# Optimization experiments

Hardware: AMD Instinct MI355X
Metric: run time of the kernel (lower is better)

## Reference

```python
import jax, jax.numpy as jnp
import numpy as np

NEG_INF = -1e9  # matches torch masked_fill value of -1000000000.0


def setup_inputs() -> dict:
    key = jax.random.key(0)
    k1, k2, k3, k4 = jax.random.split(key, 4)
    B, H, S, D = 4, 16, 2048, 128
    query = jax.random.normal(k1, (B, H, S, D), dtype=jnp.float32)
    key_t = jax.random.normal(k2, (B, H, S, D), dtype=jnp.float32)
    value = jax.random.normal(k3, (B, H, S, D), dtype=jnp.float32)
    mask = jax.random.randint(k4, (B, 1, 1, S), 0, 2, dtype=jnp.int32)
    return {"query": query, "key": key_t, "value": value, "mask": mask, "dropout": 0}


def reference(query, key, value, mask, dropout):
    # scores = Q K^T / sqrt(d_k)   [B,H,S,S]
    d_k = query.shape[-1]
    scores = jnp.einsum("bhqd,bhkd->bhqk", query, key) / jnp.sqrt(jnp.asarray(d_k, query.dtype))
    # masked_fill_(mask == 0, -1e9); mask broadcasts [B,1,1,S] -> [B,H,S,S]
    scores = jnp.where(mask == 0, jnp.asarray(NEG_INF, scores.dtype), scores)
    # dropout == 0 -> identity (deterministic reference / eval mode)
    attn = jax.nn.softmax(scores, axis=-1)
    return jnp.einsum("bhqk,bhkd->bhqd", attn, value)
```

## Files before the change

kernel.cpp:

```cpp
#include <hip/hip_runtime.h>
#include <hip/hip_bf16.h>

#define S_LEN 2048
#define D_DIM 128
#define QBLK 128
#define KVBLK 32
#define NT (S_LEN / KVBLK)
#define KCHUNK 8192
#define VCHUNK 8192
#define PRE_BYTES ((size_t)64 * NT * (KCHUNK + VCHUNK))

typedef __attribute__((ext_vector_type(8))) short short8v;
typedef __attribute__((ext_vector_type(16))) float f32x16;

static __device__ __forceinline__ unsigned f2bf2(float lo, float hi) {
    float2 f2; f2.x = lo; f2.y = hi;
    __hip_bfloat162 h2 = __float22bfloat162_rn(f2);
    unsigned r;
    __builtin_memcpy(&r, &h2, 4);
    return r;
}

static __device__ __forceinline__ void plswap(unsigned& a, unsigned& b) {
    auto r = __builtin_amdgcn_permlane32_swap(a, b, false, false);
    a = r[0]; b = r[1];
}
static __device__ __forceinline__ float plswap_sum(float x) {
    unsigned a = __float_as_uint(x), b = a;
    plswap(a, b);
    return __uint_as_float(a) + __uint_as_float(b);
}

static __device__ __forceinline__ void gload16(const void* g, void* l) {
    __builtin_amdgcn_global_load_lds(
        (const __attribute__((address_space(1))) unsigned int*)g,
        (__attribute__((address_space(3))) unsigned int*)l,
        16, 0, 0);
}

static __device__ __forceinline__ void stage8k(const unsigned char* g, unsigned char* l,
                                               int wv, int lane) {
#pragma unroll
    for (int i = 0; i < 2; ++i) {
        const int off = (wv * 2 + i) * 1024;
        gload16(g + off + lane * 16, l + off);
    }
}

#define VTS 133

__global__ __launch_bounds__(256) void preconv(
    const float* __restrict__ Kp, const float* __restrict__ Vp,
    unsigned short* __restrict__ Ko, unsigned short* __restrict__ Vo)
{
    __shared__ float vt[64 * VTS];
    const int tid = threadIdx.x;
    const int blk = blockIdx.x;
    const size_t gbase = (size_t)(blk >> 5) * S_LEN * D_DIM + (size_t)(blk & 31) * 64 * D_DIM;

#pragma unroll
    for (int i = 0; i < 8; ++i) {
        int idx = (tid + 256 * i) * 4;
        int row = idx >> 7, col = idx & 127;
        float4 v4 = *(const float4*)(Vp + gbase + idx);
        float* d = &vt[row * VTS + col];
        d[0] = v4.x; d[1] = v4.y; d[2] = v4.z; d[3] = v4.w;
    }

    unsigned short* kout = Ko + (size_t)blk * 8192;
#pragma unroll
    for (int i = 0; i < 4; ++i) {
        int o = tid + 256 * i;
        int row = o >> 4, bs = o & 15;
        int b = (bs & 8) | ((bs ^ row) & 7);
        const float* gp = Kp + gbase + row * D_DIM + 8 * b;
        float4 x = *(const float4*)gp;
        float4 y = *(const float4*)(gp + 4);
        uint4 w;
        w.x = f2bf2(x.x, x.y); w.y = f2bf2(x.z, x.w);
        w.z = f2bf2(y.x, y.y); w.w = f2bf2(y.z, y.w);
        *(uint4*)(kout + o * 8) = w;
    }
    __syncthreads();

    unsigned short* vout = Vo + (size_t)blk * 8192;
#pragma unroll
    for (int i = 0; i < 4; ++i) {
        int u = tid + 256 * i;
        int ch = u >> 9, r = u & 511;
        int d = r >> 2, bs = r & 3;
        int b = bs ^ ((d >> 1) & 3);
        const float* c0 = &vt[(ch * 32 + 8 * b) * VTS + d];
        uint4 w;
        w.x = f2bf2(c0[0 * VTS], c0[1 * VTS]);
        w.y = f2bf2(c0[2 * VTS], c0[3 * VTS]);
        w.z = f2bf2(c0[4 * VTS], c0[5 * VTS]);
        w.w = f2bf2(c0[6 * VTS], c0[7 * VTS]);
        *(uint4*)(vout + u * 8) = w;
    }
}

#define ASMEM (16384 + 16384 + 8192)

__global__ __launch_bounds__(256, 4) void sdpa_fwd_pre(
    const float* __restrict__ Qp, const unsigned short* __restrict__ Kpre,
    const unsigned short* __restrict__ Vpre, const int* __restrict__ Mp,
    float* __restrict__ Op)
{
    extern __shared__ unsigned char smem[];
    unsigned char* KbB = smem;
    unsigned char* VbB = smem + 16384;
    float* blds = (float*)(smem + 32768);

    const int tid  = threadIdx.x;
    const int lane = tid & 63;
    const int wv   = tid >> 6;
    const int h    = lane >> 5;
    const int c31  = lane & 31;
    const int hrx  = h ^ (c31 & 7);
    const int vsx  = (c31 >> 1) & 3;
    const int lbid = ((blockIdx.x & 7) << 7) | (blockIdx.x >> 3);
    const int bh   = lbid >> 4;
    const int q0   = (lbid & 15) * QBLK;
    const int bb   = bh >> 4;
    const size_t base = (size_t)bh * S_LEN * D_DIM;
    const unsigned char* Kg = (const unsigned char*)Kpre + (size_t)bh * (NT * KCHUNK);
    const unsigned char* Vg = (const unsigned char*)Vpre + (size_t)bh * (NT * VCHUNK);

    constexpr float SC   = 0.08838834764831845f * 1.4426950408889634f;
    constexpr float NEGB = -1.4426950408889634e9f;
    constexpr float M2   = 16.0f;

    {
        const int* mp = Mp + bb * S_LEN;
#pragma unroll
        for (int i = 0; i < S_LEN / 256; ++i)
            blds[tid + 256 * i] = mp[tid + 256 * i] ? -M2 : NEGB;
    }

    short8v qf[8];
    {
        const float* qrp = Qp + base + (size_t)(q0 + 32 * wv + c31) * D_DIM;
#pragma unroll
        for (int kk = 0; kk < 8; ++kk) {
            float4 x = *(const float4*)(qrp + 16 * kk + 8 * h);
            float4 y = *(const float4*)(qrp + 16 * kk + 8 * h + 4);
            uint4 w;
            w.x = f2bf2(x.x * SC, x.y * SC); w.y = f2bf2(x.z * SC, x.w * SC);
            w.z = f2bf2(y.x * SC, y.y * SC); w.w = f2bf2(y.z * SC, y.w * SC);
            *(uint4*)&qf[kk] = w;
        }
    }

    stage8k(Kg, KbB, wv, lane);
    stage8k(Vg, VbB, wv, lane);
    __syncthreads();

    f32x16 acc[4];
#pragma unroll
    for (int dt = 0; dt < 4; ++dt)
#pragma unroll
        for (int i = 0; i < 16; ++i) acc[dt][i] = 0.f;

    float lpart = 0.f;
    int cur = 0;

#pragma unroll 1
    for (int t0 = 0; t0 < NT; ++t0) {
        const unsigned char* KcB = KbB + cur * KCHUNK;
        const unsigned char* VcB = VbB + cur * VCHUNK;

        if (t0 + 1 < NT) {
            stage8k(Kg + (size_t)(t0 + 1) * KCHUNK, KbB + (cur ^ 1) * KCHUNK, wv, lane);
            stage8k(Vg + (size_t)(t0 + 1) * VCHUNK, VbB + (cur ^ 1) * VCHUNK, wv, lane);
        }

        f32x16 s;
        {
            const float* bp = blds + t0 * KVBLK + 4 * h;
#pragma unroll
            for (int t4 = 0; t4 < 4; ++t4) {
                float4 b4 = *(const float4*)(bp + 8 * t4);
                s[4 * t4 + 0] = b4.x; s[4 * t4 + 1] = b4.y;
                s[4 * t4 + 2] = b4.z; s[4 * t4 + 3] = b4.w;
            }
        }
        __builtin_amdgcn_s_setprio(1);
        {
            const unsigned char* rowp = KcB + (c31 << 8);
#pragma unroll
            for (int kk = 0; kk < 8; ++kk) {
                const int bs = ((2 * kk) & 8) | (((2 * kk) & 7) ^ hrx);
                short8v kf = *(const short8v*)(rowp + (bs << 4));
                s = __builtin_amdgcn_mfma_f32_32x32x16_bf16(kf, qf[kk], s, 0, 0, 0);
            }
        }
        __builtin_amdgcn_s_setprio(0);

        unsigned w0[4], w1[4];
#pragma unroll
        for (int t4 = 0; t4 < 4; ++t4) {
            float e0 = __builtin_amdgcn_exp2f(s[4 * t4 + 0]);
            float e1 = __builtin_amdgcn_exp2f(s[4 * t4 + 1]);
            float e2 = __builtin_amdgcn_exp2f(s[4 * t4 + 2]);
            float e3 = __builtin_amdgcn_exp2f(s[4 * t4 + 3]);
            w0[t4] = f2bf2(e0, e1);
            w1[t4] = f2bf2(e2, e3);
            lpart += (e0 + e1) + (e2 + e3);
        }

        __builtin_amdgcn_s_setprio(1);
#pragma unroll
        for (int kk = 0; kk < 2; ++kk) {
            unsigned ax = w0[2 * kk], bx = w0[2 * kk + 1];
            plswap(ax, bx);
            unsigned ay = w1[2 * kk], by = w1[2 * kk + 1];
            plswap(ay, by);
            uint4 pw;
            pw.x = ax; pw.y = ay; pw.z = bx; pw.w = by;
            short8v pfv = *(short8v*)&pw;
            const int bs = (2 * kk + h) ^ vsx;
#pragma unroll
            for (int dt = 0; dt < 4; ++dt) {
                short8v vf = *(const short8v*)(VcB + ((32 * dt + c31) << 6) + (bs << 4));
                acc[dt] = __builtin_amdgcn_mfma_f32_32x32x16_bf16(vf, pfv, acc[dt], 0, 0, 0);
            }
        }
        __builtin_amdgcn_s_setprio(0);

        __syncthreads();
        cur ^= 1;
    }

    const float linv = 1.0f / plswap_sum(lpart);
    float* sw = (float*)(smem + wv * (32 * 68 * 4));
#pragma unroll
    for (int ph = 0; ph < 2; ++ph) {
#pragma unroll
        for (int dp = 0; dp < 2; ++dp) {
            const int dtg = 2 * ph + dp;
#pragma unroll
            for (int r = 0; r < 16; ++r) {
                int dloc = 32 * dp + (r & 3) + 8 * (r >> 2) + 4 * h;
                sw[c31 * 68 + dloc] = acc[dtg][r] * linv;
            }
        }
#pragma unroll
        for (int it = 0; it < 8; ++it) {
            int f4 = lane + 64 * it;
            int qq = f4 >> 4, c4 = f4 & 15;
            float4 val = *(const float4*)&sw[qq * 68 + 4 * c4];
            *(float4*)(Op + base + (size_t)(q0 + 32 * wv + qq) * D_DIM + 64 * ph + 4 * c4) = val;
        }
    }
}

#define FBKV 64
#define FBNT (S_LEN / FBKV)
#define KSTRIDE 136
#define VSTRIDE 72
#define KELEMS (FBKV * KSTRIDE)
#define VELEMS (D_DIM * VSTRIDE)
#define KBYTES (2 * KELEMS * 2)
#define VBYTES (2 * VELEMS * 2)
#define FBSMEM (KBYTES + VBYTES + S_LEN * 4)

struct KReg { float4 a[4][2]; };
struct VReg { float4 a[2][4]; };

static __device__ __forceinline__ void load_K(KReg& kr, const float* Kbase,
                                              int kv0, int kr0, int kc8) {
#pragma unroll
    for (int i = 0; i < 4; ++i) {
        const float* gp = Kbase + (size_t)(kv0 + kr0 + 16 * i) * D_DIM + 8 * kc8;
        kr.a[i][0] = *(const float4*)gp;
        kr.a[i][1] = *(const float4*)(gp + 4);
    }
}
static __device__ __forceinline__ void write_K(const KReg& kr, unsigned short* Kn,
                                               int kr0, int kc8) {
#pragma unroll
    for (int i = 0; i < 4; ++i) {
        uint4 w;
        w.x = f2bf2(kr.a[i][0].x, kr.a[i][0].y);
        w.y = f2bf2(kr.a[i][0].z, kr.a[i][0].w);
        w.z = f2bf2(kr.a[i][1].x, kr.a[i][1].y);
        w.w = f2bf2(kr.a[i][1].z, kr.a[i][1].w);
        *(uint4*)&Kn[(kr0 + 16 * i) * KSTRIDE + 8 * kc8] = w;
    }
}
static __device__ __forceinline__ void load_V(VReg& vr, const float* Vbase,
                                              int kv0, int vkq, int vdg) {
#pragma unroll
    for (int ii = 0; ii < 2; ++ii)
#pragma unroll
        for (int r = 0; r < 4; ++r)
            vr.a[ii][r] = *(const float4*)(Vbase + (size_t)(kv0 + 4 * vkq + 32 * ii + r) * D_DIM + 4 * vdg);
}
static __device__ __forceinline__ void write_V(const VReg& vr, unsigned short* Vn,
                                               int vkq, int vdg) {
#pragma unroll
    for (int ii = 0; ii < 2; ++ii) {
        const int kvb = 4 * vkq + 32 * ii;
        const int d0  = 4 * vdg;
        uint2 u;
        u.x = f2bf2(vr.a[ii][0].x, vr.a[ii][1].x); u.y = f2bf2(vr.a[ii][2].x, vr.a[ii][3].x);
        *(uint2*)&Vn[(d0 + 0) * VSTRIDE + kvb] = u;
        u.x = f2bf2(vr.a[ii][0].y, vr.a[ii][1].y); u.y = f2bf2(vr.a[ii][2].y, vr.a[ii][3].y);
        *(uint2*)&Vn[(d0 + 1) * VSTRIDE + kvb] = u;
        u.x = f2bf2(vr.a[ii][0].z, vr.a[ii][1].z); u.y = f2bf2(vr.a[ii][2].z, vr.a[ii][3].z);
        *(uint2*)&Vn[(d0 + 2) * VSTRIDE + kvb] = u;
        u.x = f2bf2(vr.a[ii][0].w, vr.a[ii][1].w); u.y = f2bf2(vr.a[ii][2].w, vr.a[ii][3].w);
        *(uint2*)&Vn[(d0 + 3) * VSTRIDE + kvb] = u;
    }
}

__global__ __launch_bounds__(256, 2) void sdpa_fwd_fb(
    const float* __restrict__ Qp, const float* __restrict__ Kp,
    const float* __restrict__ Vp, const int* __restrict__ Mp,
    float* __restrict__ Op)
{
    extern __shared__ unsigned char smem[];
    unsigned short* Kb   = (unsigned short*)smem;
    unsigned short* Vb   = (unsigned short*)(smem + KBYTES);
    float*          mlds = (float*)(smem + KBYTES + VBYTES);

    const int tid  = threadIdx.x;
    const int lane = tid & 63;
    const int wv   = tid >> 6;
    const int h    = lane >> 5;
    const int c31  = lane & 31;
    const int bid  = blockIdx.x;
    const int bh   = bid >> 4;
    const int q0   = (bid & 15) * QBLK;
    const int bb   = bh >> 4;
    const size_t base = (size_t)bh * S_LEN * D_DIM;

    constexpr float SC   = 0.08838834764831845f * 1.4426950408889634f;
    constexpr float NEGB = -1.4426950408889634e9f;
    constexpr float THR  = 11.541560327111708f;

    {
        const int* mp = Mp + bb * S_LEN;
#pragma unroll
        for (int i = 0; i < S_LEN / 256; ++i)
            mlds[tid + 256 * i] = mp[tid + 256 * i] ? 0.f : NEGB;
    }

    short8v qf[8];
    {
        const float* qrp = Qp + base + (size_t)(q0 + 32 * wv + c31) * D_DIM;
#pragma unroll
        for (int kk = 0; kk < 8; ++kk) {
            float4 x = *(const float4*)(qrp + 16 * kk + 8 * h);
            float4 y = *(const float4*)(qrp + 16 * kk + 8 * h + 4);
            uint4 w;
            w.x = f2bf2(x.x, x.y); w.y = f2bf2(x.z, x.w);
            w.z = f2bf2(y.x, y.y); w.w = f2bf2(y.z, y.w);
            *(uint4*)&qf[kk] = w;
        }
    }

    const int kc8 = tid & 15;
    const int kr0 = tid >> 4;
    const int vdg = tid & 31;
    const int vkq = tid >> 5;

    {
        KReg kr; VReg vr;
        load_K(kr, Kp + base, 0, kr0, kc8);
        load_V(vr, Vp + base, 0, vkq, vdg);
        write_K(kr, Kb, kr0, kc8);
        write_V(vr, Vb, vkq, vdg);
    }
    __syncthreads();

    f32x16 acc[4];
#pragma unroll
    for (int dt = 0; dt < 4; ++dt)
#pragma unroll
        for (int i = 0; i < 16; ++i) acc[dt][i] = 0.f;

    float m2 = -INFINITY;
    float lsum = 0.f;
    int cur = 0;

#pragma unroll 1
    for (int t0 = 0; t0 < FBNT; ++t0) {
        const int kv0 = t0 * FBKV;
        unsigned short* Kc = Kb + cur * KELEMS;
        unsigned short* Vc = Vb + cur * VELEMS;
        unsigned short* Kn = Kb + (cur ^ 1) * KELEMS;
        unsigned short* Vn = Vb + (cur ^ 1) * VELEMS;
        const bool pf = (t0 + 1 < FBNT);

        KReg kr; VReg vr;
        if (pf) {
            load_K(kr, Kp + base, kv0 + FBKV, kr0, kc8);
            load_V(vr, Vp + base, kv0 + FBKV, vkq, vdg);
        }

        f32x16 stc[2];
        __builtin_amdgcn_s_setprio(1);
#pragma unroll
        for (int c = 0; c < 2; ++c) {
            f32x16 s;
#pragma unroll
            for (int i = 0; i < 16; ++i) s[i] = 0.f;
#pragma unroll
            for (int kk = 0; kk < 8; ++kk) {
                short8v kf = *(const short8v*)&Kc[(32 * c + c31) * KSTRIDE + 16 * kk + 8 * h];
                s = __builtin_amdgcn_mfma_f32_32x32x16_bf16(kf, qf[kk], s, 0, 0, 0);
            }
            stc[c] = s;
        }
        __builtin_amdgcn_s_setprio(0);

        float p[2][16];
#pragma unroll
        for (int c = 0; c < 2; ++c)
#pragma unroll
            for (int t = 0; t < 4; ++t) {
                float4 b4 = *(const float4*)&mlds[kv0 + 32 * c + 8 * t + 4 * h];
                p[c][4 * t + 0] = fmaf(stc[c][4 * t + 0], SC, b4.x);
                p[c][4 * t + 1] = fmaf(stc[c][4 * t + 1], SC, b4.y);
                p[c][4 * t + 2] = fmaf(stc[c][4 * t + 2], SC, b4.z);
                p[c][4 * t + 3] = fmaf(stc[c][4 * t + 3], SC, b4.w);
            }

        float pmax = -INFINITY;
#pragma unroll
        for (int c = 0; c < 2; ++c)
#pragma unroll
            for (int r = 0; r < 16; ++r) pmax = fmaxf(pmax, p[c][r]);
        pmax = fmaxf(pmax, __shfl_xor(pmax, 32));
        if (!__all(pmax <= m2 + THR)) {
            float mnew = fmaxf(m2, pmax);
            float fr = __builtin_amdgcn_exp2f(m2 - mnew);
            m2 = mnew;
            lsum *= fr;
#pragma unroll
            for (int dt = 0; dt < 4; ++dt)
#pragma unroll
                for (int i = 0; i < 16; ++i) acc[dt][i] *= fr;
        }
        float ssum = 0.f;
#pragma unroll
        for (int c = 0; c < 2; ++c)
#pragma unroll
            for (int r = 0; r < 16; ++r) {
                float e = __builtin_amdgcn_exp2f(p[c][r] - m2);
                p[c][r] = e; ssum += e;
            }
        ssum += __shfl_xor(ssum, 32);
        lsum += ssum;

        unsigned w0[2][4], w1[2][4];
#pragma unroll
        for (int c = 0; c < 2; ++c)
#pragma unroll
            for (int t = 0; t < 4; ++t) {
                w0[c][t] = f2bf2(p[c][4 * t + 0], p[c][4 * t + 1]);
                w1[c][t] = f2bf2(p[c][4 * t + 2], p[c][4 * t + 3]);
            }

        __builtin_amdgcn_s_setprio(1);
#pragma unroll
        for (int kk = 0; kk < 4; ++kk) {
            const int t0i = (2 * kk) & 3,     c0i = (2 * kk) >> 2;
            const int t1i = (2 * kk + 1) & 3, c1i = (2 * kk + 1) >> 2;
            unsigned own0 = h ? w0[c1i][t1i] : w0[c0i][t0i];
            unsigned own1 = h ? w1[c1i][t1i] : w1[c0i][t0i];
            unsigned snd0 = h ? w0[c0i][t0i] : w0[c1i][t1i];
            unsigned snd1 = h ? w1[c0i][t0i] : w1[c1i][t1i];
            unsigned r0 = __shfl_xor(snd0, 32);
            unsigned r1 = __shfl_xor(snd1, 32);
            uint4 pw;
            pw.x = h ? r0 : own0;  pw.y = h ? r1 : own1;
            pw.z = h ? own0 : r0;  pw.w = h ? own1 : r1;
            short8v pfv = *(short8v*)&pw;
#pragma unroll
            for (int dt = 0; dt < 4; ++dt) {
                short8v vf = *(const short8v*)&Vc[(32 * dt + c31) * VSTRIDE + 16 * kk + 8 * h];
                acc[dt] = __builtin_amdgcn_mfma_f32_32x32x16_bf16(vf, pfv, acc[dt], 0, 0, 0);
            }
        }
        __builtin_amdgcn_s_setprio(0);

        if (pf) {
            write_K(kr, Kn, kr0, kc8);
            write_V(vr, Vn, vkq, vdg);
        }
        __syncthreads();
        cur ^= 1;
    }

    __syncthreads();
    const float linv = 1.0f / lsum;
    float* sw = (float*)(smem + wv * (32 * 68 * 4));
#pragma unroll
    for (int ph = 0; ph < 2; ++ph) {
#pragma unroll
        for (int dp = 0; dp < 2; ++dp) {
            const int dtg = 2 * ph + dp;
#pragma unroll
            for (int r = 0; r < 16; ++r) {
                int dloc = 32 * dp + (r & 3) + 8 * (r >> 2) + 4 * h;
                sw[c31 * 68 + dloc] = acc[dtg][r] * linv;
            }
        }
#pragma unroll
        for (int it = 0; it < 8; ++it) {
            int f4 = lane + 64 * it;
            int qq = f4 >> 4, c4 = f4 & 15;
            float4 val = *(const float4*)&sw[qq * 68 + 4 * c4];
            *(float4*)(Op + base + (size_t)(q0 + 32 * wv + qq) * D_DIM + 64 * ph + 4 * c4) = val;
        }
    }
}

extern "C" void kernel_launch(void* const* d_in, const int* in_sizes, int n_in,
                              void* d_out, int out_size, void* d_ws, size_t ws_size,
                              hipStream_t stream) {
    (void)in_sizes; (void)n_in; (void)out_size;
    const float* Q = (const float*)d_in[0];
    const float* K = (const float*)d_in[1];
    const float* V = (const float*)d_in[2];
    const int*   M = (const int*)d_in[3];
    float*       O = (float*)d_out;

    if (ws_size >= PRE_BYTES) {
        unsigned short* Kpre = (unsigned short*)d_ws;
        unsigned short* Vpre = (unsigned short*)((char*)d_ws + PRE_BYTES / 2);
        hipLaunchKernelGGL(preconv, dim3(64 * 32), dim3(256), 0, stream, K, V, Kpre, Vpre);
        hipLaunchKernelGGL(sdpa_fwd_pre, dim3(1024), dim3(256), ASMEM, stream, Q, Kpre, Vpre, M, O);
    } else {
        hipLaunchKernelGGL(sdpa_fwd_fb, dim3(1024), dim3(256), FBSMEM, stream, Q, K, V, M, O);
    }
}
```

Before: 216.1 us.

## Process two 32-row query groups per wave to reuse K/V LDS fragments

Doubles the query tile per block from 128 to 256 rows, so each wave computes two 32-row query groups against the same K and V fragments read from LDS. This halves the number of blocks, each with twice the work, and cuts staging of K/V chunks into LDS per query row. In exchange, register pressure roughly doubles (two Q fragment sets, two accumulator sets), so launch bounds drop to 2 blocks per CU. With 512 blocks, occupancy and load balance across CUs may suffer.

```diff
diff --git a/kernel.cpp b/kernel.cpp
--- a/kernel.cpp
+++ b/kernel.cpp
@@ -3,7 +3,7 @@
 
 #define S_LEN 2048
 #define D_DIM 128
-#define QBLK 128
+#define QBLK 256
 #define KVBLK 32
 #define NT (S_LEN / KVBLK)
 #define KCHUNK 8192
@@ -102,7 +102,7 @@
 
 #define ASMEM (16384 + 16384 + 8192)
 
-__global__ __launch_bounds__(256, 4) void sdpa_fwd_pre(
+__global__ __launch_bounds__(256, 2) void sdpa_fwd_pre(
     const float* __restrict__ Qp, const unsigned short* __restrict__ Kpre,
     const unsigned short* __restrict__ Vpre, const int* __restrict__ Mp,
     float* __restrict__ Op)
@@ -119,9 +119,9 @@
     const int c31  = lane & 31;
     const int hrx  = h ^ (c31 & 7);
     const int vsx  = (c31 >> 1) & 3;
-    const int lbid = ((blockIdx.x & 7) << 7) | (blockIdx.x >> 3);
-    const int bh   = lbid >> 4;
-    const int q0   = (lbid & 15) * QBLK;
+    const int lbid = ((blockIdx.x & 7) << 6) | (blockIdx.x >> 3);
+    const int bh   = lbid >> 3;
+    const int q0   = (lbid & 7) * QBLK;
     const int bb   = bh >> 4;
     const size_t base = (size_t)bh * S_LEN * D_DIM;
     const unsigned char* Kg = (const unsigned char*)Kpre + (size_t)bh * (NT * KCHUNK);
@@ -138,9 +138,10 @@
             blds[tid + 256 * i] = mp[tid + 256 * i] ? -M2 : NEGB;
     }
 
-    short8v qf[8];
-    {
-        const float* qrp = Qp + base + (size_t)(q0 + 32 * wv + c31) * D_DIM;
+    short8v qf0[8], qf1[8];
+#pragma unroll
+    for (int g = 0; g < 2; ++g) {
+        const float* qrp = Qp + base + (size_t)(q0 + 64 * wv + 32 * g + c31) * D_DIM;
 #pragma unroll
         for (int kk = 0; kk < 8; ++kk) {
             float4 x = *(const float4*)(qrp + 16 * kk + 8 * h);
@@ -148,7 +149,7 @@
             uint4 w;
             w.x = f2bf2(x.x * SC, x.y * SC); w.y = f2bf2(x.z * SC, x.w * SC);
             w.z = f2bf2(y.x * SC, y.y * SC); w.w = f2bf2(y.z * SC, y.w * SC);
-            *(uint4*)&qf[kk] = w;
+            if (g == 0) *(uint4*)&qf0[kk] = w; else *(uint4*)&qf1[kk] = w;
         }
     }
 
@@ -156,13 +157,13 @@
     stage8k(Vg, VbB, wv, lane);
     __syncthreads();
 
-    f32x16 acc[4];
+    f32x16 acc0[4], acc1[4];
 #pragma unroll
     for (int dt = 0; dt < 4; ++dt)
 #pragma unroll
-        for (int i = 0; i < 16; ++i) acc[dt][i] = 0.f;
-
-    float lpart = 0.f;
+        for (int i = 0; i < 16; ++i) { acc0[dt][i] = 0.f; acc1[dt][i] = 0.f; }
+
+    float lp0 = 0.f, lp1 = 0.f;
     int cur = 0;
 
 #pragma unroll 1
@@ -175,16 +176,19 @@
             stage8k(Vg + (size_t)(t0 + 1) * VCHUNK, VbB + (cur ^ 1) * VCHUNK, wv, lane);
         }
 
-        f32x16 s;
+        f32x16 s0, s1;
         {
             const float* bp = blds + t0 * KVBLK + 4 * h;
 #pragma unroll
             for (int t4 = 0; t4 < 4; ++t4) {
                 float4 b4 = *(const float4*)(bp + 8 * t4);
-                s[4 * t4 + 0] = b4.x; s[4 * t4 + 1] = b4.y;
-                s[4 * t4 + 2] = b4.z; s[4 * t4 + 3] = b4.w;
-            }
-        }
+                s0[4 * t4 + 0] = b4.x; s0[4 * t4 + 1] = b4.y;
+                s0[4 * t4 + 2] = b4.z; s0[4 * t4 + 3] = b4.w;
+                s1[4 * t4 + 0] = b4.x; s1[4 * t4 + 1] = b4.y;
+                s1[4 * t4 + 2] = b4.z; s1[4 * t4 + 3] = b4.w;
+            }
+        }
+
         __builtin_amdgcn_s_setprio(1);
         {
             const unsigned char* rowp = KcB + (c31 << 8);
@@ -192,38 +196,52 @@
             for (int kk = 0; kk < 8; ++kk) {
                 const int bs = ((2 * kk) & 8) | (((2 * kk) & 7) ^ hrx);
                 short8v kf = *(const short8v*)(rowp + (bs << 4));
-                s = __builtin_amdgcn_mfma_f32_32x32x16_bf16(kf, qf[kk], s, 0, 0, 0);
+                s0 = __builtin_amdgcn_mfma_f32_32x32x16_bf16(kf, qf0[kk], s0, 0, 0, 0);
+                s1 = __builtin_amdgcn_mfma_f32_32x32x16_bf16(kf, qf1[kk], s1, 0, 0, 0);
             }
         }
         __builtin_amdgcn_s_setprio(0);
 
-        unsigned w0[4], w1[4];
+        unsigned w00[4], w10[4], w01[4], w11[4];
 #pragma unroll
         for (int t4 = 0; t4 < 4; ++t4) {
-            float e0 = __builtin_amdgcn_exp2f(s[4 * t4 + 0]);
-            float e1 = __builtin_amdgcn_exp2f(s[4 * t4 + 1]);
-            float e2 = __builtin_amdgcn_exp2f(s[4 * t4 + 2]);
-            float e3 = __builtin_amdgcn_exp2f(s[4 * t4 + 3]);
-            w0[t4] = f2bf2(e0, e1);
-            w1[t4] = f2bf2(e2, e3);
-            lpart += (e0 + e1) + (e2 + e3);
+            float e0 = __builtin_amdgcn_exp2f(s0[4 * t4 + 0]);
+            float e1 = __builtin_amdgcn_exp2f(s0[4 * t4 + 1]);
+            float e2 = __builtin_amdgcn_exp2f(s0[4 * t4 + 2]);
+            float e3 = __builtin_amdgcn_exp2f(s0[4 * t4 + 3]);
+            w00[t4] = f2bf2(e0, e1);
+            w10[t4] = f2bf2(e2, e3);
+            lp0 += (e0 + e1) + (e2 + e3);
+            float f0 = __builtin_amdgcn_exp2f(s1[4 * t4 + 0]);
+            float f1 = __builtin_amdgcn_exp2f(s1[4 * t4 + 1]);
+            float f2 = __builtin_amdgcn_exp2f(s1[4 * t4 + 2]);
+            float f3 = __builtin_amdgcn_exp2f(s1[4 * t4 + 3]);
+            w01[t4] = f2bf2(f0, f1);
+            w11[t4] = f2bf2(f2, f3);
+            lp1 += (f0 + f1) + (f2 + f3);
         }
 
         __builtin_amdgcn_s_setprio(1);
 #pragma unroll
         for (int kk = 0; kk < 2; ++kk) {
-            unsigned ax = w0[2 * kk], bx = w0[2 * kk + 1];
-            plswap(ax, bx);
-            unsigned ay = w1[2 * kk], by = w1[2 * kk + 1];
-            plswap(ay, by);
-            uint4 pw;
-            pw.x = ax; pw.y = ay; pw.z = bx; pw.w = by;
-            short8v pfv = *(short8v*)&pw;
+            unsigned ax0 = w00[2 * kk], bx0 = w00[2 * kk + 1];
+            plswap(ax0, bx0);
+            unsigned ay0 = w10[2 * kk], by0 = w10[2 * kk + 1];
+            plswap(ay0, by0);
+            uint4 pw0; pw0.x = ax0; pw0.y = ay0; pw0.z = bx0; pw0.w = by0;
+            short8v pf0 = *(short8v*)&pw0;
+            unsigned ax1 = w01[2 * kk], bx1 = w01[2 * kk + 1];
+            plswap(ax1, bx1);
+            unsigned ay1 = w11[2 * kk], by1 = w11[2 * kk + 1];
+            plswap(ay1, by1);
+            uint4 pw1; pw1.x = ax1; pw1.y = ay1; pw1.z = bx1; pw1.w = by1;
+            short8v pf1 = *(short8v*)&pw1;
             const int bs = (2 * kk + h) ^ vsx;
 #pragma unroll
             for (int dt = 0; dt < 4; ++dt) {
                 short8v vf = *(const short8v*)(VcB + ((32 * dt + c31) << 6) + (bs << 4));
-                acc[dt] = __builtin_amdgcn_mfma_f32_32x32x16_bf16(vf, pfv, acc[dt], 0, 0, 0);
+                acc0[dt] = __builtin_amdgcn_mfma_f32_32x32x16_bf16(vf, pf0, acc0[dt], 0, 0, 0);
+                acc1[dt] = __builtin_amdgcn_mfma_f32_32x32x16_bf16(vf, pf1, acc1[dt], 0, 0, 0);
             }
         }
         __builtin_amdgcn_s_setprio(0);
@@ -232,31 +250,40 @@
         cur ^= 1;
     }
 
-    const float linv = 1.0f / plswap_sum(lpart);
+    const float linv0 = 1.0f / plswap_sum(lp0);
+    const float linv1 = 1.0f / plswap_sum(lp1);
     float* sw = (float*)(smem + wv * (32 * 68 * 4));
-#pragma unroll
-    for (int ph = 0; ph < 2; ++ph) {
-#pragma unroll
-        for (int dp = 0; dp < 2; ++dp) {
-            const int dtg = 2 * ph + dp;
-#pragma unroll
-            for (int r = 0; r < 16; ++r) {
-                int dloc = 32 * dp + (r & 3) + 8 * (r >> 2) + 4 * h;
-                sw[c31 * 68 + dloc] = acc[dtg][r] * linv;
-            }
-        }
-#pragma unroll
-        for (int it = 0; it < 8; ++it) {
-            int f4 = lane + 64 * it;
-            int qq = f4 >> 4, c4 = f4 & 15;
-            float4 val = *(const float4*)&sw[qq * 68 + 4 * c4];
-            *(float4*)(Op + base + (size_t)(q0 + 32 * wv + qq) * D_DIM + 64 * ph + 4 * c4) = val;
-        }
-    }
+#define EPILOG(ACC, LINV, G)                                                     \
+    {                                                                            \
+        _Pragma("unroll")                                                        \
+        for (int ph = 0; ph < 2; ++ph) {                                         \
+            _Pragma("unroll")                                                    \
+            for (int dp = 0; dp < 2; ++dp) {                                     \
+                const int dtg = 2 * ph + dp;                                     \
+                _Pragma("unroll")                                                \
+                for (int r = 0; r < 16; ++r) {                                   \
+                    int dloc = 32 * dp + (r & 3) + 8 * (r >> 2) + 4 * h;         \
+                    sw[c31 * 68 + dloc] = ACC[dtg][r] * (LINV);                  \
+                }                                                                \
+            }                                                                    \
+            _Pragma("unroll")                                                    \
+            for (int it = 0; it < 8; ++it) {                                     \
+                int f4 = lane + 64 * it;                                         \
+                int qq = f4 >> 4, c4 = f4 & 15;                                  \
+                float4 val = *(const float4*)&sw[qq * 68 + 4 * c4];              \
+                *(float4*)(Op + base + (size_t)(q0 + 64 * wv + 32 * (G) + qq)    \
+                           * D_DIM + 64 * ph + 4 * c4) = val;                    \
+            }                                                                    \
+        }                                                                        \
+    }
+    EPILOG(acc0, linv0, 0)
+    EPILOG(acc1, linv1, 1)
+#undef EPILOG
 }
 
 #define FBKV 64
 #define FBNT (S_LEN / FBKV)
+#define FBQB 128
 #define KSTRIDE 136
 #define VSTRIDE 72
 #define KELEMS (FBKV * KSTRIDE)
@@ -332,7 +359,7 @@
     const int c31  = lane & 31;
     const int bid  = blockIdx.x;
     const int bh   = bid >> 4;
-    const int q0   = (bid & 15) * QBLK;
+    const int q0   = (bid & 15) * FBQB;
     const int bb   = bh >> 4;
     const size_t base = (size_t)bh * S_LEN * D_DIM;
 
@@ -533,7 +560,8 @@
         unsigned short* Kpre = (unsigned short*)d_ws;
         unsigned short* Vpre = (unsigned short*)((char*)d_ws + PRE_BYTES / 2);
         hipLaunchKernelGGL(preconv, dim3(64 * 32), dim3(256), 0, stream, K, V, Kpre, Vpre);
-        hipLaunchKernelGGL(sdpa_fwd_pre, dim3(1024), dim3(256), ASMEM, stream, Q, Kpre, Vpre, M, O);
+        hipLaunchKernelGGL(sdpa_fwd_pre, dim3(64 * (S_LEN / QBLK)), dim3(256), ASMEM, stream,
+                           Q, Kpre, Vpre, M, O);
     } else {
         hipLaunchKernelGGL(sdpa_fwd_fb, dim3(1024), dim3(256), FBSMEM, stream, Q, K, V, M, O);
     }
```

Result: faster. 201.6 us (-6.7%).

## Double KV tile to 64 keys per iteration with matching V layout

Applied to the files above, without the earlier changes.

Raises the KV block from 32 to 64 keys, so each loop iteration stages 16KB K and V chunks and issues two QK MFMAs per k-step plus four PV k-steps. The V pre-conversion layout and swizzle are rewritten to match the 64-key chunk. This halves the number of loop iterations and the barrier and prefetch overhead per key. In exchange LDS use per block doubles, occupancy drops from 4 to 3 blocks, and register pressure rises.

```diff
diff --git a/kernel.cpp b/kernel.cpp
--- a/kernel.cpp
+++ b/kernel.cpp
@@ -4,10 +4,10 @@
 #define S_LEN 2048
 #define D_DIM 128
 #define QBLK 128
-#define KVBLK 32
+#define KVBLK 64
 #define NT (S_LEN / KVBLK)
-#define KCHUNK 8192
-#define VCHUNK 8192
+#define KCHUNK 16384
+#define VCHUNK 16384
 #define PRE_BYTES ((size_t)64 * NT * (KCHUNK + VCHUNK))
 
 typedef __attribute__((ext_vector_type(8))) short short8v;
@@ -38,11 +38,11 @@
         16, 0, 0);
 }
 
-static __device__ __forceinline__ void stage8k(const unsigned char* g, unsigned char* l,
-                                               int wv, int lane) {
-#pragma unroll
-    for (int i = 0; i < 2; ++i) {
-        const int off = (wv * 2 + i) * 1024;
+static __device__ __forceinline__ void stage16k(const unsigned char* g, unsigned char* l,
+                                                int wv, int lane) {
+#pragma unroll
+    for (int i = 0; i < 4; ++i) {
+        const int off = (wv * 4 + i) * 1024;
         gload16(g + off + lane * 16, l + off);
     }
 }
@@ -56,7 +56,7 @@
     __shared__ float vt[64 * VTS];
     const int tid = threadIdx.x;
     const int blk = blockIdx.x;
-    const size_t gbase = (size_t)(blk >> 5) * S_LEN * D_DIM + (size_t)(blk & 31) * 64 * D_DIM;
+    const size_t gbase = (size_t)(blk >> 5) * S_LEN * D_DIM + (size_t)(blk & 31) * KVBLK * D_DIM;
 
 #pragma unroll
     for (int i = 0; i < 8; ++i) {
@@ -86,31 +86,30 @@
     unsigned short* vout = Vo + (size_t)blk * 8192;
 #pragma unroll
     for (int i = 0; i < 4; ++i) {
-        int u = tid + 256 * i;
-        int ch = u >> 9, r = u & 511;
-        int d = r >> 2, bs = r & 3;
-        int b = bs ^ ((d >> 1) & 3);
-        const float* c0 = &vt[(ch * 32 + 8 * b) * VTS + d];
+        int o = tid + 256 * i;
+        int d = o >> 3, bs = o & 7;
+        int b = (bs ^ d) & 7;
+        const float* c0 = &vt[(8 * b) * VTS + d];
         uint4 w;
         w.x = f2bf2(c0[0 * VTS], c0[1 * VTS]);
         w.y = f2bf2(c0[2 * VTS], c0[3 * VTS]);
         w.z = f2bf2(c0[4 * VTS], c0[5 * VTS]);
         w.w = f2bf2(c0[6 * VTS], c0[7 * VTS]);
-        *(uint4*)(vout + u * 8) = w;
-    }
-}
-
-#define ASMEM (16384 + 16384 + 8192)
-
-__global__ __launch_bounds__(256, 4) void sdpa_fwd_pre(
+        *(uint4*)(vout + o * 8) = w;
+    }
+}
+
+#define ASMEM (32768 + 32768 + 8192)
+
+__global__ __launch_bounds__(256, 3) void sdpa_fwd_pre(
     const float* __restrict__ Qp, const unsigned short* __restrict__ Kpre,
     const unsigned short* __restrict__ Vpre, const int* __restrict__ Mp,
     float* __restrict__ Op)
 {
     extern __shared__ unsigned char smem[];
     unsigned char* KbB = smem;
-    unsigned char* VbB = smem + 16384;
-    float* blds = (float*)(smem + 32768);
+    unsigned char* VbB = smem + 32768;
+    float* blds = (float*)(smem + 65536);
 
     const int tid  = threadIdx.x;
     const int lane = tid & 63;
@@ -118,7 +117,6 @@
     const int h    = lane >> 5;
     const int c31  = lane & 31;
     const int hrx  = h ^ (c31 & 7);
-    const int vsx  = (c31 >> 1) & 3;
     const int lbid = ((blockIdx.x & 7) << 7) | (blockIdx.x >> 3);
     const int bh   = lbid >> 4;
     const int q0   = (lbid & 15) * QBLK;
@@ -152,8 +150,8 @@
         }
     }
 
-    stage8k(Kg, KbB, wv, lane);
-    stage8k(Vg, VbB, wv, lane);
+    stage16k(Kg, KbB, wv, lane);
+    stage16k(Vg, VbB, wv, lane);
     __syncthreads();
 
     f32x16 acc[4];
@@ -171,58 +169,75 @@
         const unsigned char* VcB = VbB + cur * VCHUNK;
 
         if (t0 + 1 < NT) {
-            stage8k(Kg + (size_t)(t0 + 1) * KCHUNK, KbB + (cur ^ 1) * KCHUNK, wv, lane);
-            stage8k(Vg + (size_t)(t0 + 1) * VCHUNK, VbB + (cur ^ 1) * VCHUNK, wv, lane);
-        }
-
-        f32x16 s;
+            stage16k(Kg + (size_t)(t0 + 1) * KCHUNK, KbB + (cur ^ 1) * KCHUNK, wv, lane);
+            stage16k(Vg + (size_t)(t0 + 1) * VCHUNK, VbB + (cur ^ 1) * VCHUNK, wv, lane);
+        }
+
+        f32x16 sA, sB;
         {
             const float* bp = blds + t0 * KVBLK + 4 * h;
 #pragma unroll
             for (int t4 = 0; t4 < 4; ++t4) {
                 float4 b4 = *(const float4*)(bp + 8 * t4);
-                s[4 * t4 + 0] = b4.x; s[4 * t4 + 1] = b4.y;
-                s[4 * t4 + 2] = b4.z; s[4 * t4 + 3] = b4.w;
-            }
-        }
+                sA[4 * t4 + 0] = b4.x; sA[4 * t4 + 1] = b4.y;
+                sA[4 * t4 + 2] = b4.z; sA[4 * t4 + 3] = b4.w;
+                float4 b5 = *(const float4*)(bp + 32 + 8 * t4);
+                sB[4 * t4 + 0] = b5.x; sB[4 * t4 + 1] = b5.y;
+                sB[4 * t4 + 2] = b5.z; sB[4 * t4 + 3] = b5.w;
+            }
+        }
+
         __builtin_amdgcn_s_setprio(1);
         {
-            const unsigned char* rowp = KcB + (c31 << 8);
+            const unsigned char* rowpA = KcB + (c31 << 8);
+            const unsigned char* rowpB = KcB + ((32 + c31) << 8);
 #pragma unroll
             for (int kk = 0; kk < 8; ++kk) {
                 const int bs = ((2 * kk) & 8) | (((2 * kk) & 7) ^ hrx);
-                short8v kf = *(const short8v*)(rowp + (bs << 4));
-                s = __builtin_amdgcn_mfma_f32_32x32x16_bf16(kf, qf[kk], s, 0, 0, 0);
+                short8v kfA = *(const short8v*)(rowpA + (bs << 4));
+                short8v kfB = *(const short8v*)(rowpB + (bs << 4));
+                sA = __builtin_amdgcn_mfma_f32_32x32x16_bf16(kfA, qf[kk], sA, 0, 0, 0);
+                sB = __builtin_amdgcn_mfma_f32_32x32x16_bf16(kfB, qf[kk], sB, 0, 0, 0);
             }
         }
         __builtin_amdgcn_s_setprio(0);
 
-        unsigned w0[4], w1[4];
+        unsigned w0A[4], w1A[4], w0B[4], w1B[4];
 #pragma unroll
         for (int t4 = 0; t4 < 4; ++t4) {
-            float e0 = __builtin_amdgcn_exp2f(s[4 * t4 + 0]);
-            float e1 = __builtin_amdgcn_exp2f(s[4 * t4 + 1]);
-            float e2 = __builtin_amdgcn_exp2f(s[4 * t4 + 2]);
-            float e3 = __builtin_amdgcn_exp2f(s[4 * t4 + 3]);
-            w0[t4] = f2bf2(e0, e1);
-            w1[t4] = f2bf2(e2, e3);
+            float e0 = __builtin_amdgcn_exp2f(sA[4 * t4 + 0]);
+            float e1 = __builtin_amdgcn_exp2f(sA[4 * t4 + 1]);
+            float e2 = __builtin_amdgcn_exp2f(sA[4 * t4 + 2]);
+            float e3 = __builtin_amdgcn_exp2f(sA[4 * t4 + 3]);
+            w0A[t4] = f2bf2(e0, e1);
+            w1A[t4] = f2bf2(e2, e3);
             lpart += (e0 + e1) + (e2 + e3);
+            float f0 = __builtin_amdgcn_exp2f(sB[4 * t4 + 0]);
+            float f1 = __builtin_amdgcn_exp2f(sB[4 * t4 + 1]);
+            float f2 = __builtin_amdgcn_exp2f(sB[4 * t4 + 2]);
+            float f3 = __builtin_amdgcn_exp2f(sB[4 * t4 + 3]);
+            w0B[t4] = f2bf2(f0, f1);
+            w1B[t4] = f2bf2(f2, f3);
+            lpart += (f0 + f1) + (f2 + f3);
         }
 
         __builtin_amdgcn_s_setprio(1);
 #pragma unroll
-        for (int kk = 0; kk < 2; ++kk) {
-            unsigned ax = w0[2 * kk], bx = w0[2 * kk + 1];
+        for (int ks = 0; ks < 4; ++ks) {
+            const int kkl = ks & 1;
+            unsigned ax = (ks < 2) ? w0A[2 * kkl] : w0B[2 * kkl];
+            unsigned bx = (ks < 2) ? w0A[2 * kkl + 1] : w0B[2 * kkl + 1];
             plswap(ax, bx);
-            unsigned ay = w1[2 * kk], by = w1[2 * kk + 1];
+            unsigned ay = (ks < 2) ? w1A[2 * kkl] : w1B[2 * kkl];
+            unsigned by = (ks < 2) ? w1A[2 * kkl + 1] : w1B[2 * kkl + 1];
             plswap(ay, by);
             uint4 pw;
             pw.x = ax; pw.y = ay; pw.z = bx; pw.w = by;
             short8v pfv = *(short8v*)&pw;
-            const int bs = (2 * kk + h) ^ vsx;
+            const int bs = ((2 * ks) ^ hrx) & 7;
 #pragma unroll
             for (int dt = 0; dt < 4; ++dt) {
-                short8v vf = *(const short8v*)(VcB + ((32 * dt + c31) << 6) + (bs << 4));
+                short8v vf = *(const short8v*)(VcB + ((32 * dt + c31) << 7) + (bs << 4));
                 acc[dt] = __builtin_amdgcn_mfma_f32_32x32x16_bf16(vf, pfv, acc[dt], 0, 0, 0);
             }
         }
@@ -257,6 +272,7 @@
 
 #define FBKV 64
 #define FBNT (S_LEN / FBKV)
+#define FBQB 128
 #define KSTRIDE 136
 #define VSTRIDE 72
 #define KELEMS (FBKV * KSTRIDE)
@@ -332,7 +348,7 @@
     const int c31  = lane & 31;
     const int bid  = blockIdx.x;
     const int bh   = bid >> 4;
-    const int q0   = (bid & 15) * QBLK;
+    const int q0   = (bid & 15) * FBQB;
     const int bb   = bh >> 4;
     const size_t base = (size_t)bh * S_LEN * D_DIM;
 
@@ -532,8 +548,9 @@
     if (ws_size >= PRE_BYTES) {
         unsigned short* Kpre = (unsigned short*)d_ws;
         unsigned short* Vpre = (unsigned short*)((char*)d_ws + PRE_BYTES / 2);
-        hipLaunchKernelGGL(preconv, dim3(64 * 32), dim3(256), 0, stream, K, V, Kpre, Vpre);
-        hipLaunchKernelGGL(sdpa_fwd_pre, dim3(1024), dim3(256), ASMEM, stream, Q, Kpre, Vpre, M, O);
+        hipLaunchKernelGGL(preconv, dim3(64 * NT), dim3(256), 0, stream, K, V, Kpre, Vpre);
+        hipLaunchKernelGGL(sdpa_fwd_pre, dim3(64 * (S_LEN / QBLK)), dim3(256), ASMEM, stream,
+                           Q, Kpre, Vpre, M, O);
     } else {
         hipLaunchKernelGGL(sdpa_fwd_fb, dim3(1024), dim3(256), FBSMEM, stream, Q, K, V, M, O);
     }
```

Result: faster. 188.3 us (-12.9%).

## Triple-buffer K/V staging with prefetch distance two and explicit vmcnt waits

Applied to the files above, without the earlier changes.

The precomputed-bf16 attention kernel now keeps three K/V LDS buffers and prefetches two tiles ahead. The end-of-iteration __syncthreads is replaced by a partial s_waitcnt vmcnt plus a raw s_barrier, so the next tile's loads can stay in flight across the barrier. The s_setprio hints around the MFMA sections are removed in both kernels. The launch bound drops from 4 to 2 blocks per CU and LDS use grows, which may lower occupancy. The hand-written vmcnt counts depend on how stage8k issues its loads, so a wrong count risks stale data.

```diff
diff --git a/kernel.cpp b/kernel.cpp
--- a/kernel.cpp
+++ b/kernel.cpp
@@ -100,17 +100,17 @@
     }
 }
 
-#define ASMEM (16384 + 16384 + 8192)
-
-__global__ __launch_bounds__(256, 4) void sdpa_fwd_pre(
+#define ASMEM (3 * KCHUNK + 3 * VCHUNK + 8192)
+
+__global__ __launch_bounds__(256, 2) void sdpa_fwd_pre(
     const float* __restrict__ Qp, const unsigned short* __restrict__ Kpre,
     const unsigned short* __restrict__ Vpre, const int* __restrict__ Mp,
     float* __restrict__ Op)
 {
     extern __shared__ unsigned char smem[];
     unsigned char* KbB = smem;
-    unsigned char* VbB = smem + 16384;
-    float* blds = (float*)(smem + 32768);
+    unsigned char* VbB = smem + 3 * KCHUNK;
+    float* blds = (float*)(smem + 3 * KCHUNK + 3 * VCHUNK);
 
     const int tid  = threadIdx.x;
     const int lane = tid & 63;
@@ -154,7 +154,10 @@
 
     stage8k(Kg, KbB, wv, lane);
     stage8k(Vg, VbB, wv, lane);
-    __syncthreads();
+    stage8k(Kg + KCHUNK, KbB + KCHUNK, wv, lane);
+    stage8k(Vg + VCHUNK, VbB + VCHUNK, wv, lane);
+    asm volatile("s_waitcnt vmcnt(4) lgkmcnt(0)" ::: "memory");
+    __builtin_amdgcn_s_barrier();
 
     f32x16 acc[4];
 #pragma unroll
@@ -170,9 +173,11 @@
         const unsigned char* KcB = KbB + cur * KCHUNK;
         const unsigned char* VcB = VbB + cur * VCHUNK;
 
-        if (t0 + 1 < NT) {
-            stage8k(Kg + (size_t)(t0 + 1) * KCHUNK, KbB + (cur ^ 1) * KCHUNK, wv, lane);
-            stage8k(Vg + (size_t)(t0 + 1) * VCHUNK, VbB + (cur ^ 1) * VCHUNK, wv, lane);
+        const bool pf = (t0 + 2 < NT);
+        if (pf) {
+            int stg = cur + 2; if (stg >= 3) stg -= 3;
+            stage8k(Kg + (size_t)(t0 + 2) * KCHUNK, KbB + stg * KCHUNK, wv, lane);
+            stage8k(Vg + (size_t)(t0 + 2) * VCHUNK, VbB + stg * VCHUNK, wv, lane);
         }
 
         f32x16 s;
@@ -185,7 +190,7 @@
                 s[4 * t4 + 2] = b4.z; s[4 * t4 + 3] = b4.w;
             }
         }
-        __builtin_amdgcn_s_setprio(1);
+
         {
             const unsigned char* rowp = KcB + (c31 << 8);
 #pragma unroll
@@ -195,7 +200,6 @@
                 s = __builtin_amdgcn_mfma_f32_32x32x16_bf16(kf, qf[kk], s, 0, 0, 0);
             }
         }
-        __builtin_amdgcn_s_setprio(0);
 
         unsigned w0[4], w1[4];
 #pragma unroll
@@ -209,7 +213,6 @@
             lpart += (e0 + e1) + (e2 + e3);
         }
 
-        __builtin_amdgcn_s_setprio(1);
 #pragma unroll
         for (int kk = 0; kk < 2; ++kk) {
             unsigned ax = w0[2 * kk], bx = w0[2 * kk + 1];
@@ -226,10 +229,14 @@
                 acc[dt] = __builtin_amdgcn_mfma_f32_32x32x16_bf16(vf, pfv, acc[dt], 0, 0, 0);
             }
         }
-        __builtin_amdgcn_s_setprio(0);
-
-        __syncthreads();
-        cur ^= 1;
+
+        if (pf) {
+            asm volatile("s_waitcnt vmcnt(4)" ::: "memory");
+        } else {
+            asm volatile("s_waitcnt vmcnt(0)" ::: "memory");
+        }
+        __builtin_amdgcn_s_barrier();
+        cur = (cur + 1 == 3) ? 0 : cur + 1;
     }
 
     const float linv = 1.0f / plswap_sum(lpart);
@@ -257,6 +264,7 @@
 
 #define FBKV 64
 #define FBNT (S_LEN / FBKV)
+#define FBQB 128
 #define KSTRIDE 136
 #define VSTRIDE 72
 #define KELEMS (FBKV * KSTRIDE)
@@ -332,7 +340,7 @@
     const int c31  = lane & 31;
     const int bid  = blockIdx.x;
     const int bh   = bid >> 4;
-    const int q0   = (bid & 15) * QBLK;
+    const int q0   = (bid & 15) * FBQB;
     const int bb   = bh >> 4;
     const size_t base = (size_t)bh * S_LEN * D_DIM;
 
@@ -401,7 +409,6 @@
         }
 
         f32x16 stc[2];
-        __builtin_amdgcn_s_setprio(1);
 #pragma unroll
         for (int c = 0; c < 2; ++c) {
             f32x16 s;
@@ -414,7 +421,6 @@
             }
             stc[c] = s;
         }
-        __builtin_amdgcn_s_setprio(0);
 
         float p[2][16];
 #pragma unroll
@@ -464,7 +470,6 @@
                 w1[c][t] = f2bf2(p[c][4 * t + 2], p[c][4 * t + 3]);
             }
 
-        __builtin_amdgcn_s_setprio(1);
 #pragma unroll
         for (int kk = 0; kk < 4; ++kk) {
             const int t0i = (2 * kk) & 3,     c0i = (2 * kk) >> 2;
@@ -485,7 +490,6 @@
                 acc[dt] = __builtin_amdgcn_mfma_f32_32x32x16_bf16(vf, pfv, acc[dt], 0, 0, 0);
             }
         }
-        __builtin_amdgcn_s_setprio(0);
 
         if (pf) {
             write_K(kr, Kn, kr0, kc8);
@@ -533,7 +537,8 @@
         unsigned short* Kpre = (unsigned short*)d_ws;
         unsigned short* Vpre = (unsigned short*)((char*)d_ws + PRE_BYTES / 2);
         hipLaunchKernelGGL(preconv, dim3(64 * 32), dim3(256), 0, stream, K, V, Kpre, Vpre);
-        hipLaunchKernelGGL(sdpa_fwd_pre, dim3(1024), dim3(256), ASMEM, stream, Q, Kpre, Vpre, M, O);
+        hipLaunchKernelGGL(sdpa_fwd_pre, dim3(1024), dim3(256), ASMEM, stream,
+                           Q, Kpre, Vpre, M, O);
     } else {
         hipLaunchKernelGGL(sdpa_fwd_fb, dim3(1024), dim3(256), FBSMEM, stream, Q, K, V, M, O);
     }
```

Result: faster. 193.2 us (-10.6%).
